# Kernel tuning notes

Measured on AMD Instinct MI355X. Metric: run time of the kernel, lower is better.

The kernel has to match this reference:

```python
import jax, jax.numpy as jnp
import numpy as np

SEQ_LEN = 4096
N_FEAT = 2048
N_PADD = 128


def setup_inputs() -> dict:
    key = jax.random.key(0)
    kx, kw = jax.random.split(key)
    x = jax.random.normal(kx, (SEQ_LEN, N_FEAT), dtype=jnp.float32)
    # Fused QKV dense: features = 3 * n_feat
    W = jax.random.normal(kw, (N_FEAT, 3 * N_FEAT), dtype=jnp.float32) * (1.0 / np.sqrt(N_FEAT))
    b = jnp.zeros((3 * N_FEAT,), dtype=jnp.float32)
    return {"x": x, "W": W, "b": b, "n_padd": N_PADD}


def reference(x, W, b, n_padd):
    # Fused QKV projection, split along feature axis (as in nn.Dense + jnp.split)
    qkv = x @ W + b  # [S, 3F]
    q, k, v = jnp.split(qkv, 3, axis=1)  # each [S, F]
    S, F = q.shape
    idx = jnp.arange(S)
    # scores[i, j] = q_i . k_j / sqrt(F)
    scores = (q @ k.T) * (1.0 / jnp.sqrt(jnp.float32(F)))  # [S, S]
    seq_mask = idx >= n_padd                      # valid (non-padding) positions
    causal = idx[None, :] <= idx[:, None]         # j <= i
    mask = causal & seq_mask[None, :]             # kernel: causal_mask & seq_mask
    row_valid = seq_mask                          # rows < n_padd are not computed/stored
    neg_inf = jnp.float32(-jnp.inf)
    scores = jnp.where(mask, scores, neg_inf)
    # Fully-masked (padding) rows would softmax to NaN; neutralize then zero output.
    scores = jnp.where(row_valid[:, None], scores, 0.0)
    att = jax.nn.softmax(scores, axis=-1)         # row-wise stable softmax
    out = att @ v                                 # [S, F]
    out = jnp.where(row_valid[:, None], out, 0.0)  # padded rows produce zeros
    return out
```

## Files before the change

### kernel.cpp

```cpp
#include <hip/hip_runtime.h>
#include <cstdint>
#include <cstddef>
#include <cmath>

typedef unsigned short u16;
typedef short v8s __attribute__((ext_vector_type(8)));
typedef float v4f __attribute__((ext_vector_type(4)));

constexpr int SEQ = 4096;
constexpr int FEAT = 2048;
constexpr int F3 = 6144;


__device__ __forceinline__ u16 f2bf(float f) {
  union { float f; uint32_t u; } v; v.f = f;
  uint32_t r = v.u + 0x7FFFu + ((v.u >> 16) & 1u);
  return (u16)(r >> 16);
}

__device__ __forceinline__ float bf2f(u16 s) {
  union { uint32_t u; float f; } v; v.u = ((uint32_t)s) << 16;
  return v.f;
}

__device__ __forceinline__ void gld_lds16(const u16* g, u16* l) {
  __builtin_amdgcn_global_load_lds(
      (const __attribute__((address_space(1))) void*)g,
      (__attribute__((address_space(3))) void*)l, 16, 0, 0);
}


__global__ void cvt_f32_bf16(const float* __restrict__ in, u16* __restrict__ out, int n8) {
  int i = blockIdx.x * 256 + threadIdx.x;
  if (i >= n8) return;
  const float4* p = (const float4*)in + (size_t)i * 2;
  float4 a = p[0], b = p[1];
  union { u16 s[8]; uint4 v; } u;
  u.s[0] = f2bf(a.x); u.s[1] = f2bf(a.y); u.s[2] = f2bf(a.z); u.s[3] = f2bf(a.w);
  u.s[4] = f2bf(b.x); u.s[5] = f2bf(b.y); u.s[6] = f2bf(b.z); u.s[7] = f2bf(b.w);
  *(uint4*)(out + (size_t)i * 8) = u.v;
}

__global__ void transp_f2b(const float* __restrict__ in, int ldin,
                           u16* __restrict__ out, int ldout) {
  __shared__ float tile[32][33];
  int c0 = blockIdx.x * 32, r0 = blockIdx.y * 32;
  int tx = threadIdx.x, ty = threadIdx.y;
#pragma unroll
  for (int p = 0; p < 4; ++p)
    tile[ty + 8 * p][tx] = in[(size_t)(r0 + ty + 8 * p) * ldin + c0 + tx];
  __syncthreads();
#pragma unroll
  for (int p = 0; p < 4; ++p)
    out[(size_t)(c0 + ty + 8 * p) * ldout + r0 + tx] = f2bf(tile[tx][ty + 8 * p]);
}

__global__ void transp_b2b(const u16* __restrict__ in, int ldin,
                           u16* __restrict__ out, int ldout) {
  __shared__ u16 tile[32][33];
  int c0 = blockIdx.x * 32, r0 = blockIdx.y * 32;
  int tx = threadIdx.x, ty = threadIdx.y;
#pragma unroll
  for (int p = 0; p < 4; ++p)
    tile[ty + 8 * p][tx] = in[(size_t)(r0 + ty + 8 * p) * ldin + c0 + tx];
  __syncthreads();
#pragma unroll
  for (int p = 0; p < 4; ++p)
    out[(size_t)(c0 + ty + 8 * p) * ldout + r0 + tx] = tile[tx][ty + 8 * p];
}

__global__ __launch_bounds__(256) void add2_f32(
    const float* __restrict__ a, const float* __restrict__ b,
    float* __restrict__ o, int n4) {
  int i = blockIdx.x * 256 + threadIdx.x;
  if (i >= n4) return;
  float4 y = ((const float4*)b)[i];
  if (i >= 2048 * (FEAT / 4)) {
    float4 x = ((const float4*)a)[i];
    y.x += x.x; y.y += x.y; y.z += x.z; y.w += x.w;
  }
  ((float4*)o)[i] = y;
}


#define BARW() asm volatile("s_barrier" ::: "memory")
#define VMC6() asm volatile("s_waitcnt vmcnt(6)" ::: "memory")
#define LGKM0() asm volatile("s_waitcnt lgkmcnt(0)" ::: "memory")

#define STAGE(SB, KO) do { \
  u16* Lb = &LDSU[SB][0] + w * 512; \
  gld_lds16(pA0 + (KO), Lb); \
  gld_lds16(pA0 + (size_t)64 * LDA_ + (KO), Lb + 2048); \
  gld_lds16(pB0 + (KO), Lb + 4096); \
  gld_lds16(pB0 + (size_t)64 * LDB_ + (KO), Lb + 4096 + 2048); \
  gld_lds16(pB0 + (size_t)128 * LDB_ + (KO), Lb + 4096 + 4096); \
  gld_lds16(pB0 + (size_t)192 * LDB_ + (KO), Lb + 4096 + 6144); \
} while (0)

#define LOADA(BUF) do { _Pragma("unroll") \
  for (int mi = 0; mi < 8; ++mi) \
    af[mi] = *(const v8s*)(&LDSU[BUF][0] + (mi * 16 + lm) * 32 + lqs); \
} while (0)

#define LOADB(BUF) do { _Pragma("unroll") \
  for (int ni = 0; ni < 4; ++ni) \
    bf4[ni] = *(const v8s*)(&LDSU[BUF][0] + 4096 + (w * 64 + ni * 16 + lm) * 32 + lqs); \
} while (0)

template<int LDA_, int LDB_, int LDC_, int OUTMODE ,
         int ADDB, int MODE, int SWZ>
__global__ __launch_bounds__(256, 2) void gemmw(
    const u16* __restrict__ A, const u16* __restrict__ B,
    void* __restrict__ Cv, int K,
    const float* __restrict__ bias, float scale) {
  int bj;
  int sI0[2], sKs[2], sKe[2];
  float* sC[2] = {nullptr, nullptr};
  int nseg;
  if (MODE == 1) {
    const int f = blockIdx.x;
    const int p = f & 15;
    bj = (f >> 4) & 7;
    const int wi = f >> 7;
    const int d = 31 - p;
    float* p0 = (float*)Cv;
    float* p1 = p0 + (size_t)SEQ * FEAT;
    if (wi == 0) {
      nseg = 1;
      sI0[0] = d * 128; sKs[0] = 0;    sKe[0] = 2112;           sC[0] = p0;
    } else {
      nseg = 2;
      sI0[0] = d * 128; sKs[0] = 2112; sKe[0] = (d + 1) * 128;  sC[0] = p1;
      sI0[1] = p * 128; sKs[1] = 0;    sKe[1] = (p + 1) * 128;  sC[1] = p1;
    }
  } else {
    int bi;
    if (SWZ) {
      const int gx = gridDim.x, gy = gridDim.y;
      const int b = blockIdx.y * gx + blockIdx.x;
      const int cpx = (gx * gy) >> 3;
      const int s = (b & 7) * cpx + (b >> 3);
      bi = s % gy;  bj = s / gy;
    } else { bj = blockIdx.x; bi = blockIdx.y; }
    nseg = 1;
    sI0[0] = bi * 128; sKs[0] = 0; sKe[0] = K; sC[0] = nullptr;
  }
  const int j0 = bj * 256;

  __shared__ u16 LDSU[3][12288];

  const int t = threadIdx.x;
  const int w = t >> 6, l = t & 63;
  const int lm = l & 15, lq = l >> 4;
  const int lqs = ((lq + (lm >> 1)) & 3) * 8;

  const int rA = w * 16 + (l >> 2);
  const int cA = ((((l & 3) - ((rA >> 1) & 3)) & 3)) * 8;
  const u16* pB0 = B + (size_t)(j0 + rA) * LDB_ + cA;

  auto run_seg = [&](int i0, int ks, int ke, float* Cf) {
    const u16* pA0 = A + (size_t)(i0 + rA) * LDA_ + cA;

    v4f acc[8][4];
#pragma unroll
    for (int a = 0; a < 8; ++a)
#pragma unroll
      for (int b2 = 0; b2 < 4; ++b2)
        acc[a][b2] = v4f{0.f, 0.f, 0.f, 0.f};

    v8s af[8], bf4[4];

    STAGE(0, ks); STAGE(1, ks + 32);
    VMC6(); BARW();
    LOADB(0);

    const int nt = (ke - ks) >> 5;
    int b0 = 0, b1 = 1;
    for (int tt = 0; tt < nt; tt += 2) {
      const int kc = ks + (tt << 5);
      const int s2 = 3 - b0 - b1;
      {
        const int kst = (kc + 64 < ke) ? kc + 64 : ks;
        STAGE(s2, kst);
        LOADA(b0);
        __builtin_amdgcn_s_setprio(1);
#pragma unroll
        for (int mi = 0; mi < 8; ++mi)
#pragma unroll
          for (int ni = 0; ni < 4; ++ni)
            acc[mi][ni] = __builtin_amdgcn_mfma_f32_16x16x32_bf16(af[mi], bf4[ni], acc[mi][ni], 0, 0, 0);
        __builtin_amdgcn_s_setprio(0);
        VMC6(); BARW();
        LOADB(b1);
      }
      {
        const int kst = (kc + 96 < ke) ? kc + 96 : ks;
        STAGE(b0, kst);
        LOADA(b1);
        __builtin_amdgcn_s_setprio(1);
#pragma unroll
        for (int mi = 0; mi < 8; ++mi)
#pragma unroll
          for (int ni = 0; ni < 4; ++ni)
            acc[mi][ni] = __builtin_amdgcn_mfma_f32_16x16x32_bf16(af[mi], bf4[ni], acc[mi][ni], 0, 0, 0);
        __builtin_amdgcn_s_setprio(0);
        VMC6(); BARW();
        LOADB(s2);
      }
      b1 = b0; b0 = s2;
    }

#pragma unroll
    for (int mi = 0; mi < 8; ++mi) {
#pragma unroll
      for (int ni = 0; ni < 4; ++ni) {
        const int cc = j0 + w * 64 + ni * 16 + lm;
        const float badd = ADDB ? bias[cc] : 0.f;
#pragma unroll
        for (int r = 0; r < 4; ++r) {
          const int rr = i0 + mi * 16 + lq * 4 + r;
          if (OUTMODE == 0)
            ((u16*)Cv)[(size_t)rr * LDC_ + cc] = f2bf(acc[mi][ni][r] * scale + badd);
          else
            Cf[(size_t)rr * LDC_ + cc] = acc[mi][ni][r];
        }
      }
    }
  };

  run_seg(sI0[0], sKs[0], sKe[0], sC[0]);
  if (nseg == 2) run_seg(sI0[1], sKs[1], sKe[1], sC[1]);
}

#undef STAGE
#undef LOADA
#undef LOADB


#define LDA8(BUF, MH) do { _Pragma("unroll") \
  for (int fi = 0; fi < 4; ++fi) { \
    const u16* ap = &As8[BUF][wr][(MH) * 4096 + fi * 1024]; \
    af[fi][0] = *(const v8s*)(ap + off0); \
    af[fi][1] = *(const v8s*)(ap + off1); \
  } } while (0)

#define LDB8(BUF) do { _Pragma("unroll") \
  for (int ni = 0; ni < 4; ++ni) { \
    const u16* bp = &Bs8[BUF][bh][bo + ni * 1024]; \
    bfr[ni][0] = *(const v8s*)(bp + off0); \
    bfr[ni][1] = *(const v8s*)(bp + off1); \
  } } while (0)

#define MMA8(MH, NL) do { _Pragma("unroll") \
  for (int fi = 0; fi < 4; ++fi) { _Pragma("unroll") \
    for (int nn = 0; nn < 2; ++nn) { \
      acc[(MH)*4+fi][(NL)+nn] = __builtin_amdgcn_mfma_f32_16x16x32_bf16( \
          af[fi][0], bfr[(NL)+nn][0], acc[(MH)*4+fi][(NL)+nn], 0, 0, 0); \
      acc[(MH)*4+fi][(NL)+nn] = __builtin_amdgcn_mfma_f32_16x16x32_bf16( \
          af[fi][1], bfr[(NL)+nn][1], acc[(MH)*4+fi][(NL)+nn], 0, 0, 0); \
    } } } while (0)

#define STG8A(BUF, H, KO) do { \
  gld_lds16(Ag + (size_t)(H) * 128 * LDA_ + (KO), &As8[BUF][H][w8 * 1024]); \
  gld_lds16(Ag + ((size_t)(H) * 128 + 8) * LDA_ + (KO), &As8[BUF][H][w8 * 1024 + 512]); \
  } while (0)

#define STG8B(BUF, H, KO) do { \
  gld_lds16(Bg + (size_t)(H) * 128 * LDB_ + (KO), &Bs8[BUF][H][w8 * 1024]); \
  gld_lds16(Bg + ((size_t)(H) * 128 + 8) * LDB_ + (KO), &Bs8[BUF][H][w8 * 1024 + 512]); \
  } while (0)

template<int LDA_, int LDB_, int LDC_>
__global__ __launch_bounds__(512, 2) void gemm8tri(
    const u16* __restrict__ A, const u16* __restrict__ B,
    u16* __restrict__ C, int K, float scale) {
  const int b = blockIdx.x;
  const int cpx = (int)gridDim.x >> 3;
  const int s = (b & 7) * cpx + (b >> 3);
  int bi = (int)((sqrtf(8.f * s + 1.f) - 1.f) * 0.5f);
  while ((bi + 1) * (bi + 2) / 2 <= s) ++bi;
  while (bi * (bi + 1) / 2 > s) --bi;
  const int bj = s - bi * (bi + 1) / 2;
  const int i0 = bi * 256, j0 = bj * 256;

  __shared__ u16 As8[2][2][8192];
  __shared__ u16 Bs8[2][2][8192];

  const int t = threadIdx.x;
  const int w8 = t >> 6, l = t & 63;
  const int wr = w8 >> 2, wc = w8 & 3;
  const int lm = l & 15, lq = l >> 4;
  const int bh = wc >> 1, bo = (wc & 1) * 4096;

  const int off0 = lm * 64 + ((lq + lm) & 7) * 8;
  const int off1 = lm * 64 + ((lq + lm + 4) & 7) * 8;

  const int srow = w8 * 16 + (l >> 3);
  const int scol = (((l & 7) - (l >> 3)) & 7) * 8;
  const u16* Ag = A + (size_t)(i0 + srow) * LDA_ + scol;
  const u16* Bg = B + (size_t)(j0 + srow) * LDB_ + scol;

  v4f acc[8][4];
#pragma unroll
  for (int a = 0; a < 8; ++a)
#pragma unroll
    for (int b2 = 0; b2 < 4; ++b2)
      acc[a][b2] = v4f{0.f, 0.f, 0.f, 0.f};

  v8s af[4][2], bfr[4][2];

  STG8B(0, 0, 0); STG8B(0, 1, 0); STG8A(0, 0, 0); STG8A(0, 1, 0);
  STG8B(1, 0, 64); STG8B(1, 1, 64); STG8A(1, 0, 64);
  VMC6(); BARW();

  const int nit = K >> 7;
  for (int it = 0; it < nit; ++it) {
    const int kc = it << 7;
    const int k1 = kc + 64;
    int k2 = kc + 128; if (k2 >= K) k2 = 0;
    int k3 = kc + 192; if (k3 >= K) k3 = 0;

    LDA8(0, 0); LDB8(0);
    STG8A(1, 1, k1);
    BARW(); LGKM0();
    __builtin_amdgcn_s_setprio(1); MMA8(0, 0); __builtin_amdgcn_s_setprio(0);
    BARW();
    STG8B(0, 0, k2);
    BARW();
    __builtin_amdgcn_s_setprio(1); MMA8(0, 2); __builtin_amdgcn_s_setprio(0);
    BARW();
    LDA8(0, 1);
    STG8B(0, 1, k2);
    BARW(); LGKM0();
    __builtin_amdgcn_s_setprio(1); MMA8(1, 0); __builtin_amdgcn_s_setprio(0);
    BARW();
    STG8A(0, 0, k2);
    BARW();
    __builtin_amdgcn_s_setprio(1); MMA8(1, 2); __builtin_amdgcn_s_setprio(0);
    VMC6(); BARW();
    LDA8(1, 0); LDB8(1);
    STG8A(0, 1, k2);
    BARW(); LGKM0();
    __builtin_amdgcn_s_setprio(1); MMA8(0, 0); __builtin_amdgcn_s_setprio(0);
    BARW();
    STG8B(1, 0, k3);
    BARW();
    __builtin_amdgcn_s_setprio(1); MMA8(0, 2); __builtin_amdgcn_s_setprio(0);
    BARW();
    LDA8(1, 1);
    STG8B(1, 1, k3);
    BARW(); LGKM0();
    __builtin_amdgcn_s_setprio(1); MMA8(1, 0); __builtin_amdgcn_s_setprio(0);
    BARW();
    STG8A(1, 0, k3);
    BARW();
    __builtin_amdgcn_s_setprio(1); MMA8(1, 2); __builtin_amdgcn_s_setprio(0);
    VMC6(); BARW();
  }

#pragma unroll
  for (int mi = 0; mi < 8; ++mi) {
#pragma unroll
    for (int ni = 0; ni < 4; ++ni) {
      const int cc = j0 + wc * 64 + ni * 16 + lm;
#pragma unroll
      for (int r = 0; r < 4; ++r) {
        const int rr = i0 + wr * 128 + mi * 16 + lq * 4 + r;
        C[(size_t)rr * LDC_ + cc] = f2bf(acc[mi][ni][r] * scale);
      }
    }
  }
}

#undef LDA8
#undef LDB8
#undef MMA8
#undef STG8A
#undef STG8B

__global__ __launch_bounds__(256) void softmax_rows(
    const u16* __restrict__ S0,
    u16* __restrict__ att, const int* __restrict__ npad_p) {
  const int i = blockIdx.x;
  const int np = *npad_p;
  const int kend = ((i >> 7) + 1) << 7;
  const u16* r0 = S0 + (size_t)i * SEQ;
  u16* arow = att + (size_t)i * SEQ;
  const int t = threadIdx.x;
  const int w = t >> 6, l = t & 63;
  __shared__ float sm[4], ss[4];

  float m = -3.0e38f;
  for (int j0b = t * 8; j0b < kend; j0b += 2048) {
    union { u16 s8[8]; uint4 v; } ui;
    ui.v = *(const uint4*)(r0 + j0b);
#pragma unroll
    for (int q = 0; q < 8; ++q) {
      const int j = j0b + q;
      const float v = (j >= np && j <= i) ? bf2f(ui.s8[q]) : -3.0e38f;
      m = fmaxf(m, v);
    }
  }
#pragma unroll
  for (int off = 32; off > 0; off >>= 1) m = fmaxf(m, __shfl_xor(m, off));
  if (l == 0) sm[w] = m;
  __syncthreads();
  const float M = fmaxf(fmaxf(sm[0], sm[1]), fmaxf(sm[2], sm[3]));

  float s = 0.f;
  for (int j0b = t * 8; j0b < kend; j0b += 2048) {
    union { u16 s8[8]; uint4 v; } ui;
    ui.v = *(const uint4*)(r0 + j0b);
#pragma unroll
    for (int q = 0; q < 8; ++q) {
      const int j = j0b + q;
      const float v = (j >= np && j <= i) ? bf2f(ui.s8[q]) : -3.0e38f;
      s += __expf(v - M);
    }
  }
#pragma unroll
  for (int off = 32; off > 0; off >>= 1) s += __shfl_xor(s, off);
  if (l == 0) ss[w] = s;
  __syncthreads();
  const float inv = 1.f / (ss[0] + ss[1] + ss[2] + ss[3]);

  for (int j0b = t * 8; j0b < kend; j0b += 2048) {
    union { u16 s8[8]; uint4 v; } ui, uo;
    ui.v = *(const uint4*)(r0 + j0b);
#pragma unroll
    for (int q = 0; q < 8; ++q) {
      const int j = j0b + q;
      float a = 0.f;
      if (j >= np && j <= i)
        a = __expf(bf2f(ui.s8[q]) - M) * inv;
      uo.s8[q] = f2bf(a);
    }
    *(uint4*)(arow + j0b) = uo.v;
  }
}


extern "C" void kernel_launch(void* const* d_in, const int* in_sizes, int n_in,
                              void* d_out, int out_size, void* d_ws, size_t ws_size,
                              hipStream_t stream) {
  const float* x = (const float*)d_in[0];
  const float* W = (const float*)d_in[1];
  const float* b = (const float*)d_in[2];
  const int* npad = (const int*)d_in[3];
  float* out = (float*)d_out;

  char* p = (char*)d_ws;
  u16* xb = (u16*)p;
  u16* Wt = (u16*)(p + (size_t)SEQ * FEAT * 2);
  u16* att = (u16*)p;
  p += (size_t)SEQ * FEAT * 2 + (size_t)F3 * FEAT * 2;
  u16* qkvb = (u16*)p;  p += (size_t)SEQ * F3 * 2;
  u16* vt   = (u16*)p;  p += (size_t)FEAT * SEQ * 2;
  u16* sc0  = (u16*)p;  p += (size_t)SEQ * SEQ * 2;
  p += (size_t)SEQ * SEQ * 2;
  if (ws_size < (size_t)(p - (char*)d_ws)) return;

  float* p0 = (float*)sc0;
  float* p1 = p0 + (size_t)SEQ * FEAT;

  const float scale = 0.02209708691207961f;

  cvt_f32_bf16<<<SEQ * FEAT / 8 / 256, 256, 0, stream>>>(x, xb, SEQ * FEAT / 8);
  transp_f2b<<<dim3(F3 / 32, FEAT / 32), dim3(32, 8), 0, stream>>>(W, F3, Wt, FEAT);
  gemmw<FEAT, FEAT, F3, 0, 1, 0, 1><<<dim3(F3 / 256, SEQ / 128), 256, 0, stream>>>(
      xb, Wt, (void*)qkvb, FEAT, b, 1.0f);
  transp_b2b<<<dim3(FEAT / 32, SEQ / 32), dim3(32, 8), 0, stream>>>(
      qkvb + 2 * FEAT, F3, vt, SEQ);
  gemm8tri<F3, F3, SEQ><<<dim3(136), 512, 0, stream>>>(
      qkvb, qkvb + FEAT, sc0, FEAT, scale);
  softmax_rows<<<SEQ, 256, 0, stream>>>(sc0, att, npad);
  gemmw<SEQ, SEQ, FEAT, 1, 0, 1, 0><<<dim3(256), 256, 0, stream>>>(
      att, vt, (void*)p0, 0, nullptr, 1.0f);
  add2_f32<<<SEQ * FEAT / 4 / 256, 256, 0, stream>>>(p0, p1, out, SEQ * FEAT / 4);
}
```

Baseline: 376.2 us.

## Split attention-V GEMM into four K chunks with atomic accumulation into output

The att@V GEMM moves to a dedicated kernel that pairs triangle rows and splits the combined K range into four chunks of about 1024, launching 512 blocks instead of 256. Partial results are added into the zeroed output with float atomics, which removes the fp32 partial buffers and the separate add2 reduction kernel. The intent is better load balance and more CUs busy on the triangular workload. In exchange it adds a memset, atomic traffic on every output element, and a summation order that is no longer deterministic.

```diff
diff --git a/kernel.cpp b/kernel.cpp
--- a/kernel.cpp
+++ b/kernel.cpp
@@ -69,19 +69,6 @@
     out[(size_t)(c0 + ty + 8 * p) * ldout + r0 + tx] = tile[tx][ty + 8 * p];
 }
 
-__global__ __launch_bounds__(256) void add2_f32(
-    const float* __restrict__ a, const float* __restrict__ b,
-    float* __restrict__ o, int n4) {
-  int i = blockIdx.x * 256 + threadIdx.x;
-  if (i >= n4) return;
-  float4 y = ((const float4*)b)[i];
-  if (i >= 2048 * (FEAT / 4)) {
-    float4 x = ((const float4*)a)[i];
-    y.x += x.x; y.y += x.y; y.z += x.z; y.w += x.w;
-  }
-  ((float4*)o)[i] = y;
-}
-
 
 #define BARW() asm volatile("s_barrier" ::: "memory")
 #define VMC6() asm volatile("s_waitcnt vmcnt(6)" ::: "memory")
@@ -107,45 +94,17 @@
     bf4[ni] = *(const v8s*)(&LDSU[BUF][0] + 4096 + (w * 64 + ni * 16 + lm) * 32 + lqs); \
 } while (0)
 
-template<int LDA_, int LDB_, int LDC_, int OUTMODE ,
-         int ADDB, int MODE, int SWZ>
+template<int LDA_, int LDB_, int LDC_>
 __global__ __launch_bounds__(256, 2) void gemmw(
     const u16* __restrict__ A, const u16* __restrict__ B,
-    void* __restrict__ Cv, int K,
-    const float* __restrict__ bias, float scale) {
-  int bj;
-  int sI0[2], sKs[2], sKe[2];
-  float* sC[2] = {nullptr, nullptr};
-  int nseg;
-  if (MODE == 1) {
-    const int f = blockIdx.x;
-    const int p = f & 15;
-    bj = (f >> 4) & 7;
-    const int wi = f >> 7;
-    const int d = 31 - p;
-    float* p0 = (float*)Cv;
-    float* p1 = p0 + (size_t)SEQ * FEAT;
-    if (wi == 0) {
-      nseg = 1;
-      sI0[0] = d * 128; sKs[0] = 0;    sKe[0] = 2112;           sC[0] = p0;
-    } else {
-      nseg = 2;
-      sI0[0] = d * 128; sKs[0] = 2112; sKe[0] = (d + 1) * 128;  sC[0] = p1;
-      sI0[1] = p * 128; sKs[1] = 0;    sKe[1] = (p + 1) * 128;  sC[1] = p1;
-    }
-  } else {
-    int bi;
-    if (SWZ) {
-      const int gx = gridDim.x, gy = gridDim.y;
-      const int b = blockIdx.y * gx + blockIdx.x;
-      const int cpx = (gx * gy) >> 3;
-      const int s = (b & 7) * cpx + (b >> 3);
-      bi = s % gy;  bj = s / gy;
-    } else { bj = blockIdx.x; bi = blockIdx.y; }
-    nseg = 1;
-    sI0[0] = bi * 128; sKs[0] = 0; sKe[0] = K; sC[0] = nullptr;
-  }
-  const int j0 = bj * 256;
+    u16* __restrict__ C, int K,
+    const float* __restrict__ bias) {
+  const int gx = gridDim.x, gy = gridDim.y;
+  const int bb = blockIdx.y * gx + blockIdx.x;
+  const int cpx = (gx * gy) >> 3;
+  const int sw = (bb & 7) * cpx + (bb >> 3);
+  const int bi = sw % gy, bj = sw / gy;
+  const int i0 = bi * 128, j0 = bj * 256;
 
   __shared__ u16 LDSU[3][12288];
 
@@ -156,9 +115,108 @@
 
   const int rA = w * 16 + (l >> 2);
   const int cA = ((((l & 3) - ((rA >> 1) & 3)) & 3)) * 8;
+  const u16* pA0 = A + (size_t)(i0 + rA) * LDA_ + cA;
   const u16* pB0 = B + (size_t)(j0 + rA) * LDB_ + cA;
 
-  auto run_seg = [&](int i0, int ks, int ke, float* Cf) {
+  v4f acc[8][4];
+#pragma unroll
+  for (int a = 0; a < 8; ++a)
+#pragma unroll
+    for (int b2 = 0; b2 < 4; ++b2)
+      acc[a][b2] = v4f{0.f, 0.f, 0.f, 0.f};
+
+  v8s af[8], bf4[4];
+
+  STAGE(0, 0); STAGE(1, 32);
+  VMC6(); BARW();
+  LOADB(0);
+
+  const int nt = K >> 5;
+  int b0 = 0, b1 = 1;
+  for (int tt = 0; tt < nt; tt += 2) {
+    const int kc = tt << 5;
+    const int s2 = 3 - b0 - b1;
+    {
+      const int kst = (kc + 64 < K) ? kc + 64 : 0;
+      STAGE(s2, kst);
+      LOADA(b0);
+      __builtin_amdgcn_s_setprio(1);
+#pragma unroll
+      for (int mi = 0; mi < 8; ++mi)
+#pragma unroll
+        for (int ni = 0; ni < 4; ++ni)
+          acc[mi][ni] = __builtin_amdgcn_mfma_f32_16x16x32_bf16(af[mi], bf4[ni], acc[mi][ni], 0, 0, 0);
+      __builtin_amdgcn_s_setprio(0);
+      VMC6(); BARW();
+      LOADB(b1);
+    }
+    {
+      const int kst = (kc + 96 < K) ? kc + 96 : 0;
+      STAGE(b0, kst);
+      LOADA(b1);
+      __builtin_amdgcn_s_setprio(1);
+#pragma unroll
+      for (int mi = 0; mi < 8; ++mi)
+#pragma unroll
+        for (int ni = 0; ni < 4; ++ni)
+          acc[mi][ni] = __builtin_amdgcn_mfma_f32_16x16x32_bf16(af[mi], bf4[ni], acc[mi][ni], 0, 0, 0);
+      __builtin_amdgcn_s_setprio(0);
+      VMC6(); BARW();
+      LOADB(s2);
+    }
+    b1 = b0; b0 = s2;
+  }
+
+#pragma unroll
+  for (int mi = 0; mi < 8; ++mi) {
+#pragma unroll
+    for (int ni = 0; ni < 4; ++ni) {
+      const int cc = j0 + w * 64 + ni * 16 + lm;
+      const float badd = bias[cc];
+#pragma unroll
+      for (int r = 0; r < 4; ++r) {
+        const int rr = i0 + mi * 16 + lq * 4 + r;
+        C[(size_t)rr * LDC_ + cc] = f2bf(acc[mi][ni][r] + badd);
+      }
+    }
+  }
+}
+
+template<int LDA_, int LDB_, int LDC_>
+__global__ __launch_bounds__(256, 2) void attv(
+    const u16* __restrict__ A, const u16* __restrict__ B,
+    float* __restrict__ out) {
+  const int f = blockIdx.x;
+  const int p = f & 15;
+  const int bj = (f >> 4) & 7;
+  const int wi = f >> 7;
+  const int d = 31 - p;
+  const int Kd = (d + 1) * 128;
+  const int ws = wi * 1024;
+  const int we = (wi == 3) ? 4224 : ws + 1024;
+
+  int sI0[2], sKs[2], sKe[2];
+  int nseg = 0;
+  if (ws < Kd) {
+    sI0[nseg] = d * 128; sKs[nseg] = ws; sKe[nseg] = (we < Kd) ? we : Kd; ++nseg;
+  }
+  if (we > Kd) {
+    sI0[nseg] = p * 128; sKs[nseg] = (ws > Kd) ? ws - Kd : 0; sKe[nseg] = we - Kd; ++nseg;
+  }
+  const int j0 = bj * 256;
+
+  __shared__ u16 LDSU[3][12288];
+
+  const int t = threadIdx.x;
+  const int w = t >> 6, l = t & 63;
+  const int lm = l & 15, lq = l >> 4;
+  const int lqs = ((lq + (lm >> 1)) & 3) * 8;
+
+  const int rA = w * 16 + (l >> 2);
+  const int cA = ((((l & 3) - ((rA >> 1) & 3)) & 3)) * 8;
+  const u16* pB0 = B + (size_t)(j0 + rA) * LDB_ + cA;
+
+  auto run_seg = [&](int i0, int ks, int ke) {
     const u16* pA0 = A + (size_t)(i0 + rA) * LDA_ + cA;
 
     v4f acc[8][4];
@@ -215,21 +273,17 @@
 #pragma unroll
       for (int ni = 0; ni < 4; ++ni) {
         const int cc = j0 + w * 64 + ni * 16 + lm;
-        const float badd = ADDB ? bias[cc] : 0.f;
 #pragma unroll
         for (int r = 0; r < 4; ++r) {
           const int rr = i0 + mi * 16 + lq * 4 + r;
-          if (OUTMODE == 0)
-            ((u16*)Cv)[(size_t)rr * LDC_ + cc] = f2bf(acc[mi][ni][r] * scale + badd);
-          else
-            Cf[(size_t)rr * LDC_ + cc] = acc[mi][ni][r];
+          atomicAdd(out + (size_t)rr * LDC_ + cc, acc[mi][ni][r]);
         }
       }
     }
   };
 
-  run_seg(sI0[0], sKs[0], sKe[0], sC[0]);
-  if (nseg == 2) run_seg(sI0[1], sKs[1], sKe[1], sC[1]);
+  run_seg(sI0[0], sKs[0], sKe[0]);
+  if (nseg == 2) run_seg(sI0[1], sKs[1], sKe[1]);
 }
 
 #undef STAGE
@@ -457,24 +511,20 @@
   u16* qkvb = (u16*)p;  p += (size_t)SEQ * F3 * 2;
   u16* vt   = (u16*)p;  p += (size_t)FEAT * SEQ * 2;
   u16* sc0  = (u16*)p;  p += (size_t)SEQ * SEQ * 2;
-  p += (size_t)SEQ * SEQ * 2;
   if (ws_size < (size_t)(p - (char*)d_ws)) return;
 
-  float* p0 = (float*)sc0;
-  float* p1 = p0 + (size_t)SEQ * FEAT;
-
   const float scale = 0.02209708691207961f;
+
+  hipMemsetAsync(d_out, 0, (size_t)SEQ * FEAT * sizeof(float), stream);
 
   cvt_f32_bf16<<<SEQ * FEAT / 8 / 256, 256, 0, stream>>>(x, xb, SEQ * FEAT / 8);
   transp_f2b<<<dim3(F3 / 32, FEAT / 32), dim3(32, 8), 0, stream>>>(W, F3, Wt, FEAT);
-  gemmw<FEAT, FEAT, F3, 0, 1, 0, 1><<<dim3(F3 / 256, SEQ / 128), 256, 0, stream>>>(
-      xb, Wt, (void*)qkvb, FEAT, b, 1.0f);
+  gemmw<FEAT, FEAT, F3><<<dim3(F3 / 256, SEQ / 128), 256, 0, stream>>>(
+      xb, Wt, qkvb, FEAT, b);
   transp_b2b<<<dim3(FEAT / 32, SEQ / 32), dim3(32, 8), 0, stream>>>(
       qkvb + 2 * FEAT, F3, vt, SEQ);
   gemm8tri<F3, F3, SEQ><<<dim3(136), 512, 0, stream>>>(
       qkvb, qkvb + FEAT, sc0, FEAT, scale);
   softmax_rows<<<SEQ, 256, 0, stream>>>(sc0, att, npad);
-  gemmw<SEQ, SEQ, FEAT, 1, 0, 1, 0><<<dim3(256), 256, 0, stream>>>(
-      att, vt, (void*)p0, 0, nullptr, 1.0f);
-  add2_f32<<<SEQ * FEAT / 4 / 256, 256, 0, stream>>>(p0, p1, out, SEQ * FEAT / 4);
-}
+  attv<SEQ, SEQ, FEAT><<<dim3(512), 256, 0, stream>>>(att, vt, out);
+}
```

New measurement: 402.1 us. 6.9% more time.
